# Kernel optimization log

Hardware: AMD Instinct MI355X
Metric: run time of the kernel (lower is better)

## Reference

```python
import jax, jax.numpy as jnp
import numpy as np

SLOPE = 25.0   # fast_sigmoid surrogate slope
THR = 1.0      # snntorch Leaky default threshold


@jax.custom_vjp
def spike(x):
    # Heaviside forward, fast-sigmoid surrogate backward
    return (x > 0).astype(x.dtype)

def _spike_fwd(x):
    return spike(x), x

def _spike_bwd(x, g):
    return (g / (SLOPE * jnp.abs(x) + 1.0) ** 2,)

spike.defvjp(_spike_fwd, _spike_bwd)


def conv2d(x, w, b):
    y = jax.lax.conv_general_dilated(
        x, w, window_strides=(1, 1), padding=((1, 1), (1, 1)),
        dimension_numbers=('NCHW', 'OIHW', 'NCHW'))
    return y + b[None, :, None, None]


def maxpool2(x):
    return jax.lax.reduce_window(x, -jnp.inf, jax.lax.max,
                                 (1, 1, 2, 2), (1, 1, 2, 2), 'VALID')


def bn_inf(x, g, b, m, v):
    # inference-mode BatchNorm2d, eps = 1e-5
    inv = g * jax.lax.rsqrt(v + 1e-5)
    return x * inv[None, :, None, None] + (b - m * inv)[None, :, None, None]


def lif_step(mem, inp, beta):
    # snntorch Leaky, reset_mechanism='subtract', learn_beta (clamped to [0,1])
    b = jnp.clip(beta, 0.0, 1.0)
    reset = jax.lax.stop_gradient((mem > THR).astype(mem.dtype))
    mem_new = b * mem + inp - reset * THR
    spk = spike(mem_new - THR)
    return spk, mem_new


def setup_inputs() -> dict:
    key = jax.random.key(0)
    ks = jax.random.split(key, 20)
    T, B, H, W = 25, 512, 100, 64   # T steps, batch, MAX_LEN, N_MELS
    NUM_CLASSES = 35
    FLAT = 32 * (H // 4) * (W // 4)  # 12800
    f32 = jnp.float32
    inp = {
        'x': jax.random.normal(ks[0], (T, B, H, W), f32),
        'conv1_w': jax.random.normal(ks[1], (16, 1, 3, 3), f32) * 0.2,
        'conv1_b': jnp.zeros((16,), f32),
        'bn1_g': jnp.ones((16,), f32),
        'bn1_b': jnp.zeros((16,), f32),
        'bn1_m': jax.random.normal(ks[2], (16,), f32) * 0.1,
        'bn1_v': jax.random.uniform(ks[3], (16,), f32) + 0.5,
        'conv2_w': jax.random.normal(ks[4], (32, 16, 3, 3), f32) * (1.0 / np.sqrt(16 * 9)),
        'conv2_b': jnp.zeros((32,), f32),
        'bn2_g': jnp.ones((32,), f32),
        'bn2_b': jnp.zeros((32,), f32),
        'bn2_m': jax.random.normal(ks[5], (32,), f32) * 0.1,
        'bn2_v': jax.random.uniform(ks[6], (32,), f32) + 0.5,
        'fc1_w': jax.random.normal(ks[7], (256, FLAT), f32) * (1.0 / np.sqrt(FLAT)),
        'fc1_b': jnp.zeros((256,), f32),
        'fc2_w': jax.random.normal(ks[8], (128, 256), f32) * (1.0 / np.sqrt(256)),
        'fc2_b': jnp.zeros((128,), f32),
        'fc3_w': jax.random.normal(ks[9], (NUM_CLASSES, 128), f32) * (1.0 / np.sqrt(128)),
        'fc3_b': jnp.zeros((NUM_CLASSES,), f32),
        'beta1': jnp.float32(0.9),
        'beta2': jnp.float32(0.9),
        'beta3': jnp.float32(0.9),
    }
    return inp


def reference(x, conv1_w, conv1_b, bn1_g, bn1_b, bn1_m, bn1_v,
              conv2_w, conv2_b, bn2_g, bn2_b, bn2_m, bn2_v,
              fc1_w, fc1_b, fc2_w, fc2_b, fc3_w, fc3_b,
              beta1, beta2, beta3):
    T, B = x.shape[0], x.shape[1]
    # CNN runs once on the time-averaged input
    x_mean = jnp.mean(x, axis=0)[:, None]          # (B, 1, H, W)
    f = maxpool2(jax.nn.relu(bn_inf(conv2d(x_mean, conv1_w, conv1_b), bn1_g, bn1_b, bn1_m, bn1_v)))
    f = maxpool2(jax.nn.relu(bn_inf(conv2d(f, conv2_w, conv2_b), bn2_g, bn2_b, bn2_m, bn2_v)))
    feat = f.reshape(B, -1)                        # (B, FLAT)
    # fc1 input is the same every step (dropout = identity in eval)
    cur1 = feat @ fc1_w.T + fc1_b                  # (B, 256)

    m1 = jnp.zeros((B, fc1_w.shape[0]), x.dtype)
    m2 = jnp.zeros((B, fc2_w.shape[0]), x.dtype)
    m3 = jnp.zeros((B, fc3_w.shape[0]), x.dtype)

    def step(carry, _):
        m1, m2, m3 = carry
        spk1, m1 = lif_step(m1, cur1, beta1)
        spk2, m2 = lif_step(m2, spk1 @ fc2_w.T + fc2_b, beta2)
        spk3, m3 = lif_step(m3, spk2 @ fc3_w.T + fc3_b, beta3)
        return (m1, m2, m3), spk3

    _, out = jax.lax.scan(step, (m1, m2, m3), None, length=T)
    return out                                     # (T, B, NUM_CLASSES)
```

## Files before the change

kernel.cpp:

```cpp
#include <hip/hip_runtime.h>

#define N_P1    (512*16*50*32)
#define N_FEAT  (512*12800)
#define N_PART  (32*512*256)

#define WS_P1    0
#define WS_FEAT  (WS_P1 + N_P1)
#define WS_PART  (WS_FEAT + N_FEAT)
#define WS_S1    0
#define WS_IN2   3276800
#define WS_S2    4915200

__global__ __launch_bounds__(256) void conv1_kernel(const float* __restrict__ x,
                                                    const float* __restrict__ w1,
                                                    const float* __restrict__ cb1,
                                                    const float* __restrict__ g1,
                                                    const float* __restrict__ bb1,
                                                    const float* __restrict__ m1g,
                                                    const float* __restrict__ v1,
                                                    float* __restrict__ p1) {
    __shared__ float xs[22 * 66];
    __shared__ float w1s[144];
    __shared__ float sh1s[16];
    const int b = blockIdx.x, s = blockIdx.y;
    const int tid = threadIdx.x;
    if (tid < 144) {
        int c = tid / 9;
        float inv = g1[c] * rsqrtf(v1[c] + 1e-5f);
        w1s[tid] = w1[tid] * inv;
    }
    if (tid < 16) {
        float inv = g1[tid] * rsqrtf(v1[tid] + 1e-5f);
        sh1s[tid] = cb1[tid] * inv + bb1[tid] - m1g[tid] * inv;
    }
    if (tid < 44) xs[(tid >> 1) * 66 + (tid & 1) * 65] = 0.f;
    const int r0 = s * 20 - 1;
    const size_t TSTR = (size_t)512 * 6400;
    for (int i = tid; i < 22 * 16; i += 256) {
        int lr = i >> 4, cq = i & 15;
        int gr = r0 + lr;
        float4 a0 = make_float4(0.f, 0.f, 0.f, 0.f), a1 = a0, a2 = a0, a3 = a0;
        if (gr >= 0 && gr < 100) {
            const float* px = x + (size_t)b * 6400 + gr * 64 + cq * 4;
            #pragma unroll
            for (int tt = 0; tt < 24; tt += 4) {
                float4 v0 = *(const float4*)(px + (size_t)(tt + 0) * TSTR);
                float4 v1_ = *(const float4*)(px + (size_t)(tt + 1) * TSTR);
                float4 v2_ = *(const float4*)(px + (size_t)(tt + 2) * TSTR);
                float4 v3 = *(const float4*)(px + (size_t)(tt + 3) * TSTR);
                a0.x += v0.x; a0.y += v0.y; a0.z += v0.z; a0.w += v0.w;
                a1.x += v1_.x; a1.y += v1_.y; a1.z += v1_.z; a1.w += v1_.w;
                a2.x += v2_.x; a2.y += v2_.y; a2.z += v2_.z; a2.w += v2_.w;
                a3.x += v3.x; a3.y += v3.y; a3.z += v3.z; a3.w += v3.w;
            }
            float4 v = *(const float4*)(px + (size_t)24 * TSTR);
            a0.x += v.x; a0.y += v.y; a0.z += v.z; a0.w += v.w;
        }
        const float sc = 1.0f / 25.0f;
        float* d = &xs[lr * 66 + 1 + cq * 4];
        d[0] = (a0.x + a1.x + a2.x + a3.x) * sc;
        d[1] = (a0.y + a1.y + a2.y + a3.y) * sc;
        d[2] = (a0.z + a1.z + a2.z + a3.z) * sc;
        d[3] = (a0.w + a1.w + a2.w + a3.w) * sc;
    }
    __syncthreads();
    for (int pos = tid; pos < 320; pos += 256) {
        int phl = pos >> 5, pw = pos & 31;
        int ph = s * 10 + phl;
        float win[4][4];
        #pragma unroll
        for (int a = 0; a < 4; ++a)
            #pragma unroll
            for (int c2 = 0; c2 < 4; ++c2)
                win[a][c2] = xs[(2 * phl + a) * 66 + 2 * pw + c2];
        #pragma unroll 1
        for (int c = 0; c < 16; ++c) {
            float s00 = 0.f, s01 = 0.f, s10 = 0.f, s11 = 0.f;
            #pragma unroll
            for (int dh = 0; dh < 3; ++dh)
                #pragma unroll
                for (int dw = 0; dw < 3; ++dw) {
                    float w = w1s[c * 9 + dh * 3 + dw];
                    s00 = fmaf(win[dh][dw],         w, s00);
                    s01 = fmaf(win[dh][dw + 1],     w, s01);
                    s10 = fmaf(win[dh + 1][dw],     w, s10);
                    s11 = fmaf(win[dh + 1][dw + 1], w, s11);
                }
            float m = fmaxf(fmaxf(s00, s01), fmaxf(s10, s11));
            float val = fmaxf(m + sh1s[c], 0.f);
            p1[(((size_t)b * 16 + c) * 50 + ph) * 32 + pw] = val;
        }
    }
}

__global__ __launch_bounds__(320) void conv2_kernel(const float* __restrict__ p1,
                                                    const float* __restrict__ w2g,
                                                    const float* __restrict__ cb2,
                                                    const float* __restrict__ g2,
                                                    const float* __restrict__ bb2,
                                                    const float* __restrict__ m2g,
                                                    const float* __restrict__ v2,
                                                    float* __restrict__ feat) {
    __shared__ float ins[16 * 12 * 36];
    __shared__ float wl[16 * 9 * 32];
    __shared__ float sh2s[32];
    const int b = blockIdx.x, s = blockIdx.y;
    const int tid = threadIdx.x;
    const int chg = tid & 15, q = (tid >> 4) & 3, phl = tid >> 6;
    const int ph = s * 5 + phl;

    for (int i = tid; i < 192; i += 320) {
        int ci = i / 12, lr = i - ci * 12;
        int gr = s * 10 - 1 + lr;
        float* dst = &ins[(ci * 12 + lr) * 36];
        if (gr >= 0 && gr < 50) {
            const float* src = p1 + (((size_t)b * 16 + ci) * 50 + gr) * 32;
            float4 v0 = *(const float4*)src;
            dst[0] = 0.f; dst[1] = v0.x; dst[2] = v0.y; dst[3] = v0.z;
            #pragma unroll
            for (int qq = 1; qq < 8; ++qq) {
                float4 v = *(const float4*)(src + 4 * qq - 1);
                *(float4*)(dst + 4 * qq) = v;
            }
            dst[32] = src[31];
            dst[33] = 0.f; dst[34] = 0.f; dst[35] = 0.f;
        } else {
            #pragma unroll
            for (int qq = 0; qq < 9; ++qq) *(float4*)(dst + 4 * qq) = make_float4(0.f, 0.f, 0.f, 0.f);
        }
    }
    for (int i = tid; i < 4608; i += 320) {
        int c = i / 144, rem = i - c * 144;
        float inv = g2[c] * rsqrtf(v2[c] + 1e-5f);
        wl[rem * 32 + c] = w2g[i] * inv;
    }
    if (tid < 32) {
        float inv = g2[tid] * rsqrtf(v2[tid] + 1e-5f);
        sh2s[tid] = cb2[tid] * inv + bb2[tid] - m2g[tid] * inv;
    }
    __syncthreads();

    float acc[2][2][8];
    #pragma unroll
    for (int c = 0; c < 2; ++c)
        #pragma unroll
        for (int a = 0; a < 2; ++a)
            #pragma unroll
            for (int xx = 0; xx < 8; ++xx) acc[c][a][xx] = 0.f;
    const int xb = q * 8;
    #pragma unroll 1
    for (int ci = 0; ci < 16; ++ci) {
        float2 wv[9];
        #pragma unroll
        for (int t = 0; t < 9; ++t)
            wv[t] = *(const float2*)&wl[(ci * 9 + t) * 32 + 2 * chg];
        #pragma unroll
        for (int lr4 = 0; lr4 < 4; ++lr4) {
            const float* row = &ins[(ci * 12 + (2 * phl + lr4)) * 36 + xb];
            float v[10];
            float4 t0 = *(const float4*)&row[0];
            float4 t1 = *(const float4*)&row[4];
            float2 t2 = *(const float2*)&row[8];
            v[0]=t0.x; v[1]=t0.y; v[2]=t0.z; v[3]=t0.w;
            v[4]=t1.x; v[5]=t1.y; v[6]=t1.z; v[7]=t1.w;
            v[8]=t2.x; v[9]=t2.y;
            #pragma unroll
            for (int a = 0; a < 2; ++a) {
                const int dh = lr4 - a;
                if (dh >= 0 && dh <= 2) {
                    #pragma unroll
                    for (int dw = 0; dw < 3; ++dw) {
                        float w0 = wv[dh * 3 + dw].x;
                        float w1 = wv[dh * 3 + dw].y;
                        #pragma unroll
                        for (int xx = 0; xx < 8; ++xx) {
                            acc[0][a][xx] = fmaf(v[xx + dw], w0, acc[0][a][xx]);
                            acc[1][a][xx] = fmaf(v[xx + dw], w1, acc[1][a][xx]);
                        }
                    }
                }
            }
        }
    }
    #pragma unroll
    for (int ch = 0; ch < 2; ++ch) {
        const int c = 2 * chg + ch;
        const float sh = sh2s[c];
        #pragma unroll
        for (int p = 0; p < 4; ++p) {
            float m = fmaxf(fmaxf(acc[ch][0][2 * p], acc[ch][0][2 * p + 1]),
                            fmaxf(acc[ch][1][2 * p], acc[ch][1][2 * p + 1]));
            float val = fmaxf(m + sh, 0.f);
            feat[(((size_t)b * 32 + c) * 25 + ph) * 16 + q * 4 + p] = val;
        }
    }
}

__global__ __launch_bounds__(256) void fc1_kernel(const float* __restrict__ feat,
                                                  const float* __restrict__ w,
                                                  float* __restrict__ part) {
    __shared__ float As[16 * 68];
    __shared__ float Bs[16 * 136];
    const int bx = blockIdx.x, by = blockIdx.y, bz = blockIdx.z;
    const int tid = threadIdx.x;
    const int tm = tid >> 4, tn = tid & 15;
    const int r = tid >> 2, cq = tid & 3;
    const int m0 = bx * 64, n0 = by * 128;
    const size_t aBase = (size_t)(m0 + r) * 12800 + bz * 400 + cq * 4;
    const size_t bBase = (size_t)(n0 + r) * 12800 + bz * 400 + cq * 4;
    float acc[4][8];
    #pragma unroll
    for (int i = 0; i < 4; ++i)
        #pragma unroll
        for (int j = 0; j < 8; ++j) acc[i][j] = 0.f;

    for (int kt = 0; kt < 25; ++kt) {
        float4 a0 = *(const float4*)(feat + aBase + kt * 16);
        float4 b0 = *(const float4*)(w    + bBase + kt * 16);
        float4 b1 = *(const float4*)(w    + bBase + (size_t)64 * 12800 + kt * 16);
        __syncthreads();
        As[(cq * 4 + 0) * 68 + r] = a0.x; As[(cq * 4 + 1) * 68 + r] = a0.y;
        As[(cq * 4 + 2) * 68 + r] = a0.z; As[(cq * 4 + 3) * 68 + r] = a0.w;
        Bs[(cq * 4 + 0) * 136 + r]      = b0.x; Bs[(cq * 4 + 1) * 136 + r]      = b0.y;
        Bs[(cq * 4 + 2) * 136 + r]      = b0.z; Bs[(cq * 4 + 3) * 136 + r]      = b0.w;
        Bs[(cq * 4 + 0) * 136 + 64 + r] = b1.x; Bs[(cq * 4 + 1) * 136 + 64 + r] = b1.y;
        Bs[(cq * 4 + 2) * 136 + 64 + r] = b1.z; Bs[(cq * 4 + 3) * 136 + 64 + r] = b1.w;
        __syncthreads();
        #pragma unroll
        for (int kk = 0; kk < 16; ++kk) {
            float4 av  = *(const float4*)&As[kk * 68 + tm * 4];
            float4 bv0 = *(const float4*)&Bs[kk * 136 + tn * 8];
            float4 bv1 = *(const float4*)&Bs[kk * 136 + tn * 8 + 4];
            float a_[4] = {av.x, av.y, av.z, av.w};
            float b_[8] = {bv0.x, bv0.y, bv0.z, bv0.w, bv1.x, bv1.y, bv1.z, bv1.w};
            #pragma unroll
            for (int i = 0; i < 4; ++i)
                #pragma unroll
                for (int j = 0; j < 8; ++j)
                    acc[i][j] = fmaf(a_[i], b_[j], acc[i][j]);
        }
    }
    #pragma unroll
    for (int i = 0; i < 4; ++i) {
        float* dst = &part[(size_t)bz * 131072 + (size_t)(m0 + tm * 4 + i) * 256 + n0 + tn * 8];
        *(float4*)dst       = make_float4(acc[i][0], acc[i][1], acc[i][2], acc[i][3]);
        *(float4*)(dst + 4) = make_float4(acc[i][4], acc[i][5], acc[i][6], acc[i][7]);
    }
}

__global__ __launch_bounds__(256) void lif1_kernel(const float* __restrict__ part,
                                                   const float* __restrict__ b1g,
                                                   const float* __restrict__ pb1,
                                                   float* __restrict__ S1) {
    const int i = blockIdx.x * 256 + threadIdx.x;
    const int k = i & 255;
    float cu = b1g[k];
    #pragma unroll 8
    for (int z = 0; z < 32; ++z) cu += part[(size_t)z * 131072 + i];
    const float be = fminf(fmaxf(pb1[0], 0.f), 1.f);
    float m = 0.f;
    #pragma unroll
    for (int t = 0; t < 25; ++t) {
        float r = (m > 1.f) ? 1.f : 0.f;
        m = fmaf(be, m, cu) - r;
        S1[(size_t)t * 131072 + i] = (m > 1.f) ? 1.f : 0.f;
    }
}

__global__ __launch_bounds__(256) void fc2g_kernel(const float* __restrict__ S1,
                                                   const float* __restrict__ w2g,
                                                   const float* __restrict__ b2g,
                                                   float* __restrict__ in2) {
    __shared__ float As[16 * 36];
    __shared__ float Bs[16 * 136];
    const int m0 = blockIdx.x * 32;
    const int tid = threadIdx.x;
    const int tm = tid >> 4, tn = tid & 15;
    float acc[2][8];
    #pragma unroll
    for (int i = 0; i < 2; ++i)
        #pragma unroll
        for (int j = 0; j < 8; ++j) acc[i][j] = 0.f;

    for (int kt = 0; kt < 16; ++kt) {
        float4 av = make_float4(0.f, 0.f, 0.f, 0.f);
        if (tid < 128) {
            int r = tid >> 2, cq = tid & 3;
            av = *(const float4*)&S1[(size_t)(m0 + r) * 256 + kt * 16 + cq * 4];
        }
        int rb = tid >> 1, kb = (tid & 1) * 8;
        float4 bv0 = *(const float4*)&w2g[rb * 256 + kt * 16 + kb];
        float4 bv1 = *(const float4*)&w2g[rb * 256 + kt * 16 + kb + 4];
        __syncthreads();
        if (tid < 128) {
            int r = tid >> 2, cq = tid & 3;
            As[(cq * 4 + 0) * 36 + r] = av.x; As[(cq * 4 + 1) * 36 + r] = av.y;
            As[(cq * 4 + 2) * 36 + r] = av.z; As[(cq * 4 + 3) * 36 + r] = av.w;
        }
        Bs[(kb + 0) * 136 + rb] = bv0.x; Bs[(kb + 1) * 136 + rb] = bv0.y;
        Bs[(kb + 2) * 136 + rb] = bv0.z; Bs[(kb + 3) * 136 + rb] = bv0.w;
        Bs[(kb + 4) * 136 + rb] = bv1.x; Bs[(kb + 5) * 136 + rb] = bv1.y;
        Bs[(kb + 6) * 136 + rb] = bv1.z; Bs[(kb + 7) * 136 + rb] = bv1.w;
        __syncthreads();
        #pragma unroll
        for (int kk = 0; kk < 16; ++kk) {
            float2 a2 = *(const float2*)&As[kk * 36 + tm * 2];
            float4 bv0_ = *(const float4*)&Bs[kk * 136 + tn * 8];
            float4 bv1_ = *(const float4*)&Bs[kk * 136 + tn * 8 + 4];
            float b_[8] = {bv0_.x, bv0_.y, bv0_.z, bv0_.w, bv1_.x, bv1_.y, bv1_.z, bv1_.w};
            #pragma unroll
            for (int j = 0; j < 8; ++j) {
                acc[0][j] = fmaf(a2.x, b_[j], acc[0][j]);
                acc[1][j] = fmaf(a2.y, b_[j], acc[1][j]);
            }
        }
    }
    float4 bb0 = *(const float4*)&b2g[tn * 8];
    float4 bb1 = *(const float4*)&b2g[tn * 8 + 4];
    #pragma unroll
    for (int i = 0; i < 2; ++i) {
        float* dst = &in2[(size_t)(m0 + tm * 2 + i) * 128 + tn * 8];
        *(float4*)dst       = make_float4(acc[i][0] + bb0.x, acc[i][1] + bb0.y,
                                          acc[i][2] + bb0.z, acc[i][3] + bb0.w);
        *(float4*)(dst + 4) = make_float4(acc[i][4] + bb1.x, acc[i][5] + bb1.y,
                                          acc[i][6] + bb1.z, acc[i][7] + bb1.w);
    }
}

__global__ __launch_bounds__(256) void lif2_kernel(const float* __restrict__ in2,
                                                   const float* __restrict__ pb2,
                                                   float* __restrict__ S2) {
    const int i = blockIdx.x * 256 + threadIdx.x;
    const float be = fminf(fmaxf(pb2[0], 0.f), 1.f);
    float m = 0.f;
    #pragma unroll
    for (int t = 0; t < 25; ++t) {
        float r = (m > 1.f) ? 1.f : 0.f;
        m = fmaf(be, m, in2[(size_t)t * 65536 + i]) - r;
        S2[(size_t)t * 65536 + i] = (m > 1.f) ? 1.f : 0.f;
    }
}

__global__ __launch_bounds__(64) void fc3l_kernel(const float* __restrict__ S2,
                                                  const float* __restrict__ w3g,
                                                  const float* __restrict__ b3g,
                                                  const float* __restrict__ pb3,
                                                  float* __restrict__ out) {
    __shared__ float w3T[128 * 36];
    __shared__ float s2row[128];
    const int b = blockIdx.x;
    const int lane = threadIdx.x;
    for (int i = lane; i < 4480; i += 64) {
        int j = i >> 7, k = i & 127;
        w3T[k * 36 + j] = w3g[i];
    }
    const float be = fminf(fmaxf(pb3[0], 0.f), 1.f);
    const float bias = (lane < 35) ? b3g[lane] : 0.f;
    float m = 0.f;
    __syncthreads();
    for (int t = 0; t < 25; ++t) {
        float2 v = *(const float2*)&S2[(size_t)t * 65536 + b * 128 + lane * 2];
        *(float2*)&s2row[lane * 2] = v;
        __syncthreads();
        if (lane < 35) {
            float a = bias;
            #pragma unroll 8
            for (int k = 0; k < 128; ++k)
                a = fmaf(s2row[k], w3T[k * 36 + lane], a);
            float r = (m > 1.f) ? 1.f : 0.f;
            m = fmaf(be, m, a) - r;
            out[((size_t)t * 512 + b) * 35 + lane] = (m > 1.f) ? 1.f : 0.f;
        }
        __syncthreads();
    }
}

extern "C" void kernel_launch(void* const* d_in, const int* in_sizes, int n_in,
                              void* d_out, int out_size, void* d_ws, size_t ws_size,
                              hipStream_t stream) {
    const float* x     = (const float*)d_in[0];
    const float* c1w   = (const float*)d_in[1];
    const float* c1b   = (const float*)d_in[2];
    const float* bn1g  = (const float*)d_in[3];
    const float* bn1b  = (const float*)d_in[4];
    const float* bn1m  = (const float*)d_in[5];
    const float* bn1v  = (const float*)d_in[6];
    const float* c2w   = (const float*)d_in[7];
    const float* c2b   = (const float*)d_in[8];
    const float* bn2g  = (const float*)d_in[9];
    const float* bn2b  = (const float*)d_in[10];
    const float* bn2m  = (const float*)d_in[11];
    const float* bn2v  = (const float*)d_in[12];
    const float* fc1w  = (const float*)d_in[13];
    const float* fc1b  = (const float*)d_in[14];
    const float* fc2w  = (const float*)d_in[15];
    const float* fc2b  = (const float*)d_in[16];
    const float* fc3w  = (const float*)d_in[17];
    const float* fc3b  = (const float*)d_in[18];
    const float* beta1 = (const float*)d_in[19];
    const float* beta2 = (const float*)d_in[20];
    const float* beta3 = (const float*)d_in[21];
    float* ws  = (float*)d_ws;
    float* out = (float*)d_out;

    conv1_kernel<<<dim3(512, 5), 256, 0, stream>>>(x, c1w, c1b, bn1g, bn1b, bn1m, bn1v,
                                                   ws + WS_P1);
    conv2_kernel<<<dim3(512, 5), 320, 0, stream>>>(ws + WS_P1, c2w, c2b, bn2g, bn2b, bn2m, bn2v,
                                                   ws + WS_FEAT);
    fc1_kernel<<<dim3(8, 2, 32), 256, 0, stream>>>(ws + WS_FEAT, fc1w, ws + WS_PART);
    lif1_kernel<<<512, 256, 0, stream>>>(ws + WS_PART, fc1b, beta1, ws + WS_S1);
    fc2g_kernel<<<400, 256, 0, stream>>>(ws + WS_S1, fc2w, fc2b, ws + WS_IN2);
    lif2_kernel<<<256, 256, 0, stream>>>(ws + WS_IN2, beta2, ws + WS_S2);
    fc3l_kernel<<<512, 64, 0, stream>>>(ws + WS_S2, fc3w, fc3b, beta3, out);
}
```

Baseline: 328.0 us.

## Fuse fc2, LIF2, fc3 and LIF3 into one per-batch tail kernel

```diff
diff --git a/kernel.cpp b/kernel.cpp
--- a/kernel.cpp
+++ b/kernel.cpp
@@ -8,10 +8,8 @@
 #define WS_FEAT  (WS_P1 + N_P1)
 #define WS_PART  (WS_FEAT + N_FEAT)
 #define WS_S1    0
-#define WS_IN2   3276800
-#define WS_S2    4915200
-
-__global__ __launch_bounds__(256) void conv1_kernel(const float* __restrict__ x,
+
+__global__ __launch_bounds__(384) void conv1_kernel(const float* __restrict__ x,
                                                     const float* __restrict__ w1,
                                                     const float* __restrict__ cb1,
                                                     const float* __restrict__ g1,
@@ -29,15 +27,19 @@
         float inv = g1[c] * rsqrtf(v1[c] + 1e-5f);
         w1s[tid] = w1[tid] * inv;
     }
-    if (tid < 16) {
-        float inv = g1[tid] * rsqrtf(v1[tid] + 1e-5f);
-        sh1s[tid] = cb1[tid] * inv + bb1[tid] - m1g[tid] * inv;
-    }
-    if (tid < 44) xs[(tid >> 1) * 66 + (tid & 1) * 65] = 0.f;
+    if (tid >= 144 && tid < 160) {
+        int c = tid - 144;
+        float inv = g1[c] * rsqrtf(v1[c] + 1e-5f);
+        sh1s[c] = cb1[c] * inv + bb1[c] - m1g[c] * inv;
+    }
+    if (tid >= 160 && tid < 204) {
+        int q = tid - 160;
+        xs[(q >> 1) * 66 + (q & 1) * 65] = 0.f;
+    }
     const int r0 = s * 20 - 1;
     const size_t TSTR = (size_t)512 * 6400;
-    for (int i = tid; i < 22 * 16; i += 256) {
-        int lr = i >> 4, cq = i & 15;
+    if (tid < 352) {
+        int lr = tid >> 4, cq = tid & 15;
         int gr = r0 + lr;
         float4 a0 = make_float4(0.f, 0.f, 0.f, 0.f), a1 = a0, a2 = a0, a3 = a0;
         if (gr >= 0 && gr < 100) {
@@ -64,8 +66,8 @@
         d[3] = (a0.w + a1.w + a2.w + a3.w) * sc;
     }
     __syncthreads();
-    for (int pos = tid; pos < 320; pos += 256) {
-        int phl = pos >> 5, pw = pos & 31;
+    if (tid < 320) {
+        int phl = tid >> 5, pw = tid & 31;
         int ph = s * 10 + phl;
         float win[4][4];
         #pragma unroll
@@ -254,124 +256,111 @@
                                                    float* __restrict__ S1) {
     const int i = blockIdx.x * 256 + threadIdx.x;
     const int k = i & 255;
+    const int b = i >> 8;
     float cu = b1g[k];
     #pragma unroll 8
     for (int z = 0; z < 32; ++z) cu += part[(size_t)z * 131072 + i];
     const float be = fminf(fmaxf(pb1[0], 0.f), 1.f);
     float m = 0.f;
+    float* dst = S1 + (size_t)b * 6400 + k;
     #pragma unroll
     for (int t = 0; t < 25; ++t) {
         float r = (m > 1.f) ? 1.f : 0.f;
         m = fmaf(be, m, cu) - r;
-        S1[(size_t)t * 131072 + i] = (m > 1.f) ? 1.f : 0.f;
-    }
-}
-
-__global__ __launch_bounds__(256) void fc2g_kernel(const float* __restrict__ S1,
+        dst[t * 256] = (m > 1.f) ? 1.f : 0.f;
+    }
+}
+
+__global__ __launch_bounds__(320) void tail_kernel(const float* __restrict__ S1,
                                                    const float* __restrict__ w2g,
                                                    const float* __restrict__ b2g,
-                                                   float* __restrict__ in2) {
-    __shared__ float As[16 * 36];
-    __shared__ float Bs[16 * 136];
-    const int m0 = blockIdx.x * 32;
+                                                   const float* __restrict__ w3g,
+                                                   const float* __restrict__ b3g,
+                                                   const float* __restrict__ pb2,
+                                                   const float* __restrict__ pb3,
+                                                   float* __restrict__ out) {
+    __shared__ float s1L[25 * 256];
+    __shared__ float w2T[32 * 133];
+    __shared__ float w3T[128 * 36];
+    __shared__ float in2L[25 * 128];
+    __shared__ float a3L[25 * 36];
+    const int b = blockIdx.x;
     const int tid = threadIdx.x;
-    const int tm = tid >> 4, tn = tid & 15;
-    float acc[2][8];
-    #pragma unroll
-    for (int i = 0; i < 2; ++i)
-        #pragma unroll
-        for (int j = 0; j < 8; ++j) acc[i][j] = 0.f;
-
-    for (int kt = 0; kt < 16; ++kt) {
-        float4 av = make_float4(0.f, 0.f, 0.f, 0.f);
-        if (tid < 128) {
-            int r = tid >> 2, cq = tid & 3;
-            av = *(const float4*)&S1[(size_t)(m0 + r) * 256 + kt * 16 + cq * 4];
-        }
-        int rb = tid >> 1, kb = (tid & 1) * 8;
-        float4 bv0 = *(const float4*)&w2g[rb * 256 + kt * 16 + kb];
-        float4 bv1 = *(const float4*)&w2g[rb * 256 + kt * 16 + kb + 4];
+    const int tm = tid >> 6;
+    const int tn = tid & 63;
+
+    for (int i = tid; i < 1600; i += 320)
+        *(float4*)&s1L[i * 4] = *(const float4*)&S1[(size_t)b * 6400 + i * 4];
+    for (int i = tid; i < 4480; i += 320) {
+        int c = i >> 7, k = i & 127;
+        w3T[k * 36 + c] = w3g[i];
+    }
+
+    float acc[5][2];
+    #pragma unroll
+    for (int i = 0; i < 5; ++i) { acc[i][0] = 0.f; acc[i][1] = 0.f; }
+
+    #pragma unroll 1
+    for (int kt = 0; kt < 8; ++kt) {
         __syncthreads();
-        if (tid < 128) {
-            int r = tid >> 2, cq = tid & 3;
-            As[(cq * 4 + 0) * 36 + r] = av.x; As[(cq * 4 + 1) * 36 + r] = av.y;
-            As[(cq * 4 + 2) * 36 + r] = av.z; As[(cq * 4 + 3) * 36 + r] = av.w;
-        }
-        Bs[(kb + 0) * 136 + rb] = bv0.x; Bs[(kb + 1) * 136 + rb] = bv0.y;
-        Bs[(kb + 2) * 136 + rb] = bv0.z; Bs[(kb + 3) * 136 + rb] = bv0.w;
-        Bs[(kb + 4) * 136 + rb] = bv1.x; Bs[(kb + 5) * 136 + rb] = bv1.y;
-        Bs[(kb + 6) * 136 + rb] = bv1.z; Bs[(kb + 7) * 136 + rb] = bv1.w;
+        for (int i = tid; i < 4096; i += 320) {
+            int j = i >> 5, kk = i & 31;
+            w2T[kk * 133 + j] = w2g[j * 256 + kt * 32 + kk];
+        }
         __syncthreads();
         #pragma unroll
-        for (int kk = 0; kk < 16; ++kk) {
-            float2 a2 = *(const float2*)&As[kk * 36 + tm * 2];
-            float4 bv0_ = *(const float4*)&Bs[kk * 136 + tn * 8];
-            float4 bv1_ = *(const float4*)&Bs[kk * 136 + tn * 8 + 4];
-            float b_[8] = {bv0_.x, bv0_.y, bv0_.z, bv0_.w, bv1_.x, bv1_.y, bv1_.z, bv1_.w};
-            #pragma unroll
-            for (int j = 0; j < 8; ++j) {
-                acc[0][j] = fmaf(a2.x, b_[j], acc[0][j]);
-                acc[1][j] = fmaf(a2.y, b_[j], acc[1][j]);
+        for (int kk = 0; kk < 32; ++kk) {
+            float2 wv = *(const float2*)&w2T[kk * 133 + 2 * tn];
+            const float* ap = &s1L[tm * 5 * 256 + kt * 32 + kk];
+            #pragma unroll
+            for (int i = 0; i < 5; ++i) {
+                float a = ap[i * 256];
+                acc[i][0] = fmaf(a, wv.x, acc[i][0]);
+                acc[i][1] = fmaf(a, wv.y, acc[i][1]);
             }
         }
     }
-    float4 bb0 = *(const float4*)&b2g[tn * 8];
-    float4 bb1 = *(const float4*)&b2g[tn * 8 + 4];
-    #pragma unroll
-    for (int i = 0; i < 2; ++i) {
-        float* dst = &in2[(size_t)(m0 + tm * 2 + i) * 128 + tn * 8];
-        *(float4*)dst       = make_float4(acc[i][0] + bb0.x, acc[i][1] + bb0.y,
-                                          acc[i][2] + bb0.z, acc[i][3] + bb0.w);
-        *(float4*)(dst + 4) = make_float4(acc[i][4] + bb1.x, acc[i][5] + bb1.y,
-                                          acc[i][6] + bb1.z, acc[i][7] + bb1.w);
-    }
-}
-
-__global__ __launch_bounds__(256) void lif2_kernel(const float* __restrict__ in2,
-                                                   const float* __restrict__ pb2,
-                                                   float* __restrict__ S2) {
-    const int i = blockIdx.x * 256 + threadIdx.x;
-    const float be = fminf(fmaxf(pb2[0], 0.f), 1.f);
-    float m = 0.f;
-    #pragma unroll
-    for (int t = 0; t < 25; ++t) {
-        float r = (m > 1.f) ? 1.f : 0.f;
-        m = fmaf(be, m, in2[(size_t)t * 65536 + i]) - r;
-        S2[(size_t)t * 65536 + i] = (m > 1.f) ? 1.f : 0.f;
-    }
-}
-
-__global__ __launch_bounds__(64) void fc3l_kernel(const float* __restrict__ S2,
-                                                  const float* __restrict__ w3g,
-                                                  const float* __restrict__ b3g,
-                                                  const float* __restrict__ pb3,
-                                                  float* __restrict__ out) {
-    __shared__ float w3T[128 * 36];
-    __shared__ float s2row[128];
-    const int b = blockIdx.x;
-    const int lane = threadIdx.x;
-    for (int i = lane; i < 4480; i += 64) {
-        int j = i >> 7, k = i & 127;
-        w3T[k * 36 + j] = w3g[i];
-    }
-    const float be = fminf(fmaxf(pb3[0], 0.f), 1.f);
-    const float bias = (lane < 35) ? b3g[lane] : 0.f;
-    float m = 0.f;
+    {
+        float2 bias = *(const float2*)&b2g[2 * tn];
+        #pragma unroll
+        for (int i = 0; i < 5; ++i) {
+            int t = tm * 5 + i;
+            *(float2*)&in2L[t * 128 + 2 * tn] = make_float2(acc[i][0] + bias.x,
+                                                            acc[i][1] + bias.y);
+        }
+    }
     __syncthreads();
-    for (int t = 0; t < 25; ++t) {
-        float2 v = *(const float2*)&S2[(size_t)t * 65536 + b * 128 + lane * 2];
-        *(float2*)&s2row[lane * 2] = v;
-        __syncthreads();
-        if (lane < 35) {
-            float a = bias;
-            #pragma unroll 8
-            for (int k = 0; k < 128; ++k)
-                a = fmaf(s2row[k], w3T[k * 36 + lane], a);
+    if (tid < 128) {
+        const float be2 = fminf(fmaxf(pb2[0], 0.f), 1.f);
+        float m = 0.f;
+        #pragma unroll
+        for (int t = 0; t < 25; ++t) {
             float r = (m > 1.f) ? 1.f : 0.f;
-            m = fmaf(be, m, a) - r;
-            out[((size_t)t * 512 + b) * 35 + lane] = (m > 1.f) ? 1.f : 0.f;
-        }
-        __syncthreads();
+            m = fmaf(be2, m, in2L[t * 128 + tid]) - r;
+            in2L[t * 128 + tid] = (m > 1.f) ? 1.f : 0.f;
+        }
+    }
+    __syncthreads();
+    for (int i = tid; i < 875; i += 320) {
+        int t = i / 35, c = i - t * 35;
+        float a = b3g[c];
+        const float* sp = &in2L[t * 128];
+        const float* wp = &w3T[c];
+        #pragma unroll 8
+        for (int k = 0; k < 128; ++k)
+            a = fmaf(sp[k], wp[k * 36], a);
+        a3L[t * 36 + c] = a;
+    }
+    __syncthreads();
+    if (tid < 35) {
+        const float be3 = fminf(fmaxf(pb3[0], 0.f), 1.f);
+        float m = 0.f;
+        #pragma unroll
+        for (int t = 0; t < 25; ++t) {
+            float r = (m > 1.f) ? 1.f : 0.f;
+            m = fmaf(be3, m, a3L[t * 36 + tid]) - r;
+            out[((size_t)t * 512 + b) * 35 + tid] = (m > 1.f) ? 1.f : 0.f;
+        }
     }
 }
 
@@ -403,13 +392,12 @@
     float* ws  = (float*)d_ws;
     float* out = (float*)d_out;
 
-    conv1_kernel<<<dim3(512, 5), 256, 0, stream>>>(x, c1w, c1b, bn1g, bn1b, bn1m, bn1v,
+    conv1_kernel<<<dim3(512, 5), 384, 0, stream>>>(x, c1w, c1b, bn1g, bn1b, bn1m, bn1v,
                                                    ws + WS_P1);
     conv2_kernel<<<dim3(512, 5), 320, 0, stream>>>(ws + WS_P1, c2w, c2b, bn2g, bn2b, bn2m, bn2v,
                                                    ws + WS_FEAT);
     fc1_kernel<<<dim3(8, 2, 32), 256, 0, stream>>>(ws + WS_FEAT, fc1w, ws + WS_PART);
     lif1_kernel<<<512, 256, 0, stream>>>(ws + WS_PART, fc1b, beta1, ws + WS_S1);
-    fc2g_kernel<<<400, 256, 0, stream>>>(ws + WS_S1, fc2w, fc2b, ws + WS_IN2);
-    lif2_kernel<<<256, 256, 0, stream>>>(ws + WS_IN2, beta2, ws + WS_S2);
-    fc3l_kernel<<<512, 64, 0, stream>>>(ws + WS_S2, fc3w, fc3b, beta3, out);
-}
+    tail_kernel<<<512, 320, 0, stream>>>(ws + WS_S1, fc2w, fc2b, fc3w, fc3b,
+                                         beta2, beta3, out);
+}
```

New measurement: 349.7 us. 6.6% more time.
